# Kernel tuning notes

Hardware: AMD Instinct MI355X
Metric: run time of the kernel (lower is better)

The kernel has to match this reference:

```python
import jax, jax.numpy as jnp
import numpy as np

N_NODES = 100_000
N_EDGES = 1_200_000


def _lap_weights(src, dst, attr, n):
    # PyG get_laplacian(sym) + ChebConv scaling with lambda_max=2.0:
    # L_hat = (2/lmax)(I - D^-1/2 A D^-1/2) - I = -D^-1/2 A D^-1/2 (zero diagonal)
    deg = jnp.zeros((n,), attr.dtype).at[src].add(attr)
    dis = jnp.where(deg > 0, jax.lax.rsqrt(jnp.maximum(deg, 1e-30)), 0.0)
    return -(dis[src] * attr * dis[dst])


def _prop(x, src, dst, lw, n):
    # y_i = sum_{(j->i)} lw_e * x_j   (gather -> scale -> scatter-add)
    return jnp.zeros((n, x.shape[1]), x.dtype).at[dst].add(lw[:, None] * x[src])


def _cheb(x, src, dst, lw, W, b):
    # W: [K, F_in, F_out]; Tx0 = x, Tx1 = L_hat x (K<=2 here)
    out = x @ W[0]
    if W.shape[0] > 1:
        tx1 = _prop(x, src, dst, lw, x.shape[0])
        out = out + tx1 @ W[1]
    return out + b


def setup_inputs() -> dict:
    key = jax.random.key(0)
    ks = jax.random.split(key, 11)
    x = jax.random.normal(ks[0], (N_NODES, 20), jnp.float32)
    edge_index = jax.random.randint(ks[1], (2, N_EDGES), 0, N_NODES, jnp.int32)
    attr = jax.random.uniform(ks[2], (N_EDGES,), jnp.float32)
    def glorot(k, shape):
        fan = shape[-2] + shape[-1]
        return jax.random.normal(k, shape, jnp.float32) * jnp.sqrt(2.0 / fan)
    return {
        "x": x, "edge_index": edge_index, "attr": attr,
        "w1": glorot(ks[3], (1, 20, 32)), "b1": jnp.zeros((32,), jnp.float32),
        "w2": glorot(ks[4], (2, 32, 64)), "b2": jnp.zeros((64,), jnp.float32),
        "w3": glorot(ks[5], (2, 64, 2)), "b3": jnp.zeros((2,), jnp.float32),
        "gate_w": glorot(ks[6], (2, 1)), "gate_b": jnp.zeros((1,), jnp.float32),
    }


def reference(x, edge_index, attr, w1, b1, w2, b2, w3, b3, gate_w, gate_b):
    n = x.shape[0]
    src, dst = edge_index[0], edge_index[1]
    lw = _lap_weights(src, dst, attr, n)
    h = jax.nn.leaky_relu(_cheb(x, src, dst, lw, w1, b1))   # [N, 32]
    h = jax.nn.leaky_relu(_cheb(h, src, dst, lw, w2, b2))   # [N, 64]
    h = _cheb(h, src, dst, lw, w3, b3)                       # [N, 2]
    # GlobalAttention with batch = zeros (single graph): softmax over nodes
    gate = jax.nn.softmax(h @ gate_w + gate_b, axis=0)       # [N, 1]
    pooled = jnp.sum(gate * h, axis=0, keepdims=True)        # [1, 2]
    return jax.nn.log_softmax(pooled, axis=1)
```

## Files before the change

kernel.cpp:

```cpp
#include <hip/hip_runtime.h>
#include <hip/hip_bf16.h>
#include <math.h>

#define N_NODES 100000
#define N_EDGES 1200000
#define E4 (N_EDGES / 4)
#define G2B ((N_NODES + 255) / 256)
#define NB_L1 G2B
#define RANGE 12800
#define NRANGE 8
#define CHK 32
#define NB_DEG (NRANGE * CHK)
#define GPC ((E4 + CHK - 1) / CHK)
#define NBIN 391
#define BINCAP 3584
#define NB_P1 256
#define GP1 ((E4 + NB_P1 - 1) / NB_P1)

__device__ __forceinline__ float disf(float d) {
    return (d > 0.f) ? rsqrtf(d) : 0.f;
}
__device__ __forceinline__ unsigned packe(int s, float w) {
    unsigned q = (unsigned)(w * 32767.f + 0.5f);
    return ((unsigned)s << 15) | q;
}
__device__ __forceinline__ void unpacke(unsigned p, int& s, float& w) {
    s = (int)(p >> 15);
    w = (float)(p & 0x7FFFu) * (1.f / 32767.f);
}

__global__ void degbin_kernel(const int4* __restrict__ src4, const float4* __restrict__ attr4,
                              float* __restrict__ partial) {
    __shared__ float ldeg[RANGE];
    int rb = blockIdx.x;
    int r = rb / CHK;
    int c = rb - r * CHK;
    int base = r * RANGE;
    for (int j = threadIdx.x; j < RANGE; j += blockDim.x) ldeg[j] = 0.f;
    __syncthreads();
    int g0 = c * GPC;
    int g1 = g0 + GPC; if (g1 > E4) g1 = E4;
    for (int g = g0 + threadIdx.x; g < g1; g += blockDim.x) {
        int4 s = src4[g];
        float4 a = attr4[g];
        unsigned o;
        o = (unsigned)(s.x - base); if (o < RANGE) atomicAdd(&ldeg[o], a.x);
        o = (unsigned)(s.y - base); if (o < RANGE) atomicAdd(&ldeg[o], a.y);
        o = (unsigned)(s.z - base); if (o < RANGE) atomicAdd(&ldeg[o], a.z);
        o = (unsigned)(s.w - base); if (o < RANGE) atomicAdd(&ldeg[o], a.w);
    }
    __syncthreads();
    float* dstp = partial + (size_t)rb * RANGE;
    for (int j = threadIdx.x; j < RANGE; j += blockDim.x) dstp[j] = ldeg[j];
}

__global__ void degred_kernel(const float* __restrict__ partial, float* __restrict__ deg) {
    int i = blockIdx.x * blockDim.x + threadIdx.x;
    if (i >= N_NODES) return;
    int r = i / RANGE;
    int j = i - r * RANGE;
    const float* p = partial + (size_t)r * CHK * RANGE + j;
    float s = 0.f;
#pragma unroll
    for (int c = 0; c < CHK; c++) s += p[(size_t)c * RANGE];
    deg[i] = s;
}

__global__ void p1l1_kernel(const int4* __restrict__ src4, const int4* __restrict__ dst4,
                            const float4* __restrict__ attr4, const float* __restrict__ deg,
                            const float* __restrict__ x, const float* __restrict__ w1,
                            const float* __restrict__ b1,
                            int* __restrict__ binCursor, uint2* __restrict__ binRegion,
                            signed char* __restrict__ h1q, float* __restrict__ sscale) {
    __shared__ int lhist[NBIN];
    __shared__ int lbase[NBIN];
    __shared__ int lcnt[NBIN];
    __shared__ float sw[20 * 32];
    __shared__ float sb[32];

    if (blockIdx.x < NB_P1) {
        int g0 = blockIdx.x * GP1;
        int g1 = g0 + GP1; if (g1 > E4) g1 = E4;
        for (int j = threadIdx.x; j < NBIN; j += blockDim.x) { lhist[j] = 0; lcnt[j] = 0; }
        __syncthreads();
        for (int g = g0 + threadIdx.x; g < g1; g += blockDim.x) {
            int4 d = dst4[g];
            atomicAdd(&lhist[d.x >> 8], 1);
            atomicAdd(&lhist[d.y >> 8], 1);
            atomicAdd(&lhist[d.z >> 8], 1);
            atomicAdd(&lhist[d.w >> 8], 1);
        }
        __syncthreads();
        for (int j = threadIdx.x; j < NBIN; j += blockDim.x)
            lbase[j] = (lhist[j] > 0) ? atomicAdd(&binCursor[j], lhist[j]) : 0;
        __syncthreads();
        for (int g = g0 + threadIdx.x; g < g1; g += blockDim.x) {
            int4 s = src4[g];
            int4 d = dst4[g];
            float4 a = attr4[g];
            {
                int bin = d.x >> 8;
                float w = a.x * disf(deg[s.x]);
                int pos = lbase[bin] + atomicAdd(&lcnt[bin], 1);
                if (pos < BINCAP)
                    binRegion[(size_t)bin * BINCAP + pos] =
                        make_uint2(((unsigned)s.x << 8) | (unsigned)(d.x & 255), __float_as_uint(w));
            }
            {
                int bin = d.y >> 8;
                float w = a.y * disf(deg[s.y]);
                int pos = lbase[bin] + atomicAdd(&lcnt[bin], 1);
                if (pos < BINCAP)
                    binRegion[(size_t)bin * BINCAP + pos] =
                        make_uint2(((unsigned)s.y << 8) | (unsigned)(d.y & 255), __float_as_uint(w));
            }
            {
                int bin = d.z >> 8;
                float w = a.z * disf(deg[s.z]);
                int pos = lbase[bin] + atomicAdd(&lcnt[bin], 1);
                if (pos < BINCAP)
                    binRegion[(size_t)bin * BINCAP + pos] =
                        make_uint2(((unsigned)s.z << 8) | (unsigned)(d.z & 255), __float_as_uint(w));
            }
            {
                int bin = d.w >> 8;
                float w = a.w * disf(deg[s.w]);
                int pos = lbase[bin] + atomicAdd(&lcnt[bin], 1);
                if (pos < BINCAP)
                    binRegion[(size_t)bin * BINCAP + pos] =
                        make_uint2(((unsigned)s.w << 8) | (unsigned)(d.w & 255), __float_as_uint(w));
            }
        }
    } else {
        for (int t = threadIdx.x; t < 20 * 32; t += blockDim.x) sw[t] = w1[t];
        if (threadIdx.x < 32) sb[threadIdx.x] = b1[threadIdx.x];
        __syncthreads();
        int i = (blockIdx.x - NB_P1) * blockDim.x + threadIdx.x;
        if (i >= N_NODES) return;
        float xr[20];
#pragma unroll
        for (int k = 0; k < 20; k++) xr[k] = x[(size_t)i * 20 + k];
        float row[32];
        float rmax = 0.f;
#pragma unroll
        for (int j = 0; j < 32; j++) {
            float a = sb[j];
#pragma unroll
            for (int k = 0; k < 20; k++) a += xr[k] * sw[k * 32 + j];
            a = (a > 0.f) ? a : 0.01f * a;
            row[j] = a;
            rmax = fmaxf(rmax, fabsf(a));
        }
        float sc = (rmax > 0.f) ? rmax * (1.f / 127.f) : 1.f;
        float inv = (rmax > 0.f) ? 127.f / rmax : 0.f;
        sscale[i] = sc;
#pragma unroll
        for (int j = 0; j < 32; j++) {
            float q = row[j] * inv;
            h1q[(size_t)i * 32 + j] = (signed char)lrintf(q);
        }
    }
}

__global__ void binscan_kernel(const int* __restrict__ binCursor, int* __restrict__ bin_start) {
    __shared__ int sm[512];
    int t = threadIdx.x;
    int v = 0;
    if (t < NBIN) {
        v = binCursor[t];
        if (v > BINCAP) v = BINCAP;
    }
    sm[t] = v;
    __syncthreads();
    for (int off = 1; off < 512; off <<= 1) {
        int u = (t >= off) ? sm[t - off] : 0;
        __syncthreads();
        sm[t] += u;
        __syncthreads();
    }
    if (t < NBIN) bin_start[t + 1] = sm[t];
    if (t == 0) bin_start[0] = 0;
}

__global__ void p2_kernel(const uint2* __restrict__ binRegion, const int* __restrict__ bin_start,
                          int* __restrict__ row_start, unsigned* __restrict__ csr) {
    __shared__ uint2 recs[BINCAP];
    __shared__ int hist[256];
    __shared__ int excl[256];
    __shared__ int cnt[256];
    int b = blockIdx.x;
    int t = threadIdx.x;
    int base = bin_start[b];
    int c = bin_start[b + 1] - base;
    const uint2* reg = binRegion + (size_t)b * BINCAP;
    for (int j = t; j < c; j += 256) recs[j] = reg[j];
    hist[t] = 0; cnt[t] = 0;
    __syncthreads();
    for (int j = t; j < c; j += 256) atomicAdd(&hist[recs[j].x & 255u], 1);
    __syncthreads();
    int v = hist[t];
    excl[t] = v;
    __syncthreads();
    for (int off = 1; off < 256; off <<= 1) {
        int u = (t >= off) ? excl[t - off] : 0;
        __syncthreads();
        excl[t] += u;
        __syncthreads();
    }
    int ex = excl[t] - v;
    row_start[b * 256 + t] = base + ex;
    if (b == NBIN - 1 && t == 255) row_start[NBIN * 256] = bin_start[NBIN];
    __syncthreads();
    hist[t] = ex;
    __syncthreads();
    for (int j = t; j < c; j += 256) {
        unsigned w0 = recs[j].x;
        int low = (int)(w0 & 255u);
        int src = (int)(w0 >> 8);
        float w = __uint_as_float(recs[j].y);
        int pos = hist[low] + atomicAdd(&cnt[low], 1);
        csr[base + pos] = packe(src, w);
    }
}

__global__ void gl2_kernel(const int* __restrict__ row_start, const unsigned* __restrict__ csr,
                           const float* __restrict__ deg, const signed char* __restrict__ h1q,
                           const float* __restrict__ sscale,
                           const float* __restrict__ w2, const float* __restrict__ b2,
                           const float* __restrict__ w3,
                           float2* __restrict__ z0, float2* __restrict__ z1) {
    __shared__ float s0[32 * 64];
    __shared__ float s1[32 * 64];
    __shared__ float sw3[256];
    __shared__ float sb[64];
    __shared__ float h1s[8][32];
    __shared__ float t1s[8][32];
    for (int t = threadIdx.x; t < 32 * 64; t += blockDim.x) {
        s0[t] = w2[t];
        s1[t] = w2[32 * 64 + t];
    }
    for (int t = threadIdx.x; t < 256; t += blockDim.x) sw3[t] = w3[t];
    if (threadIdx.x < 64) sb[threadIdx.x] = b2[threadIdx.x];
    __syncthreads();

    int grp = threadIdx.x >> 5;
    int f   = threadIdx.x & 31;
    int node = blockIdx.x * 8 + grp;
    bool alive = (node < N_NODES);

    if (alive) {
        float hv = sscale[node] * (float)h1q[(size_t)node * 32 + f];
        int rs = row_start[node], re = row_start[node + 1];
        float acc0 = 0.f, acc1 = 0.f;
        int j = rs;
        for (; j + 1 < re; j += 2) {
            unsigned e0 = csr[j], e1 = csr[j + 1];
            int sa, sbi; float w0, w1v;
            unpacke(e0, sa, w0);
            unpacke(e1, sbi, w1v);
            float ws0 = w0 * sscale[sa];
            float ws1 = w1v * sscale[sbi];
            acc0 += ws0 * (float)h1q[(size_t)sa * 32 + f];
            acc1 += ws1 * (float)h1q[(size_t)sbi * 32 + f];
        }
        if (j < re) {
            unsigned e0 = csr[j];
            int sa; float w0;
            unpacke(e0, sa, w0);
            acc0 += w0 * sscale[sa] * (float)h1q[(size_t)sa * 32 + f];
        }
        h1s[grp][f] = hv;
        t1s[grp][f] = -disf(deg[node]) * (acc0 + acc1);
    }
    __syncthreads();

    float a0 = sb[f], a1 = sb[f + 32];
#pragma unroll 8
    for (int k = 0; k < 32; k++) {
        float h = h1s[grp][k];
        float tv = t1s[grp][k];
        a0 += h * s0[k * 64 + f]      + tv * s1[k * 64 + f];
        a1 += h * s0[k * 64 + f + 32] + tv * s1[k * 64 + f + 32];
    }
    float v0 = (a0 > 0.f) ? a0 : 0.01f * a0;
    float v1 = (a1 > 0.f) ? a1 : 0.01f * a1;

    float z00 = v0 * sw3[f * 2 + 0] + v1 * sw3[(f + 32) * 2 + 0];
    float z01 = v0 * sw3[f * 2 + 1] + v1 * sw3[(f + 32) * 2 + 1];
    float z10 = v0 * sw3[128 + f * 2 + 0] + v1 * sw3[128 + (f + 32) * 2 + 0];
    float z11 = v0 * sw3[128 + f * 2 + 1] + v1 * sw3[128 + (f + 32) * 2 + 1];
#pragma unroll
    for (int m = 16; m > 0; m >>= 1) {
        z00 += __shfl_xor(z00, m);
        z01 += __shfl_xor(z01, m);
        z10 += __shfl_xor(z10, m);
        z11 += __shfl_xor(z11, m);
    }
    if (alive && f == 0) {
        z0[node] = make_float2(z00, z01);
        z1[node] = make_float2(z10, z11);
    }
}

__global__ void g2acc_kernel(const int* __restrict__ row_start, const unsigned* __restrict__ csr,
                             const float* __restrict__ deg,
                             const float2* __restrict__ z0, const float2* __restrict__ z1,
                             const float* __restrict__ b3, const float* __restrict__ gw,
                             const float* __restrict__ gb, float4* __restrict__ quads) {
    __shared__ float sm[256], ss[256], s0[256], s1[256];
    int t = threadIdx.x;
    int i = blockIdx.x * blockDim.x + t;
    float m = -INFINITY, se = 0.f, a0 = 0.f, a1 = 0.f;
    if (i < N_NODES) {
        int rs = row_start[i], re = row_start[i + 1];
        float acc0 = 0.f, acc1 = 0.f;
        for (int j = rs; j < re; j++) {
            int s; float w;
            unpacke(csr[j], s, w);
            float2 zv = z1[s];
            acc0 += w * zv.x;
            acc1 += w * zv.y;
        }
        float di = -disf(deg[i]);
        float2 z0v = z0[i];
        float o0 = z0v.x + di * acc0 + b3[0];
        float o1 = z0v.y + di * acc1 + b3[1];
        m = o0 * gw[0] + o1 * gw[1] + gb[0];
        se = 1.f; a0 = o0; a1 = o1;
    }
    sm[t] = m; ss[t] = se; s0[t] = a0; s1[t] = a1;
    __syncthreads();
    for (int s = 128; s > 0; s >>= 1) {
        if (t < s) {
            float mb = sm[t + s];
            if (mb != -INFINITY) {
                float ma = sm[t];
                if (ma == -INFINITY) {
                    sm[t] = mb; ss[t] = ss[t + s]; s0[t] = s0[t + s]; s1[t] = s1[t + s];
                } else if (mb <= ma) {
                    float c = __expf(mb - ma);
                    ss[t] += ss[t + s] * c;
                    s0[t] += s0[t + s] * c;
                    s1[t] += s1[t + s] * c;
                } else {
                    float c = __expf(ma - mb);
                    ss[t] = ss[t] * c + ss[t + s];
                    s0[t] = s0[t] * c + s0[t + s];
                    s1[t] = s1[t] * c + s1[t + s];
                    sm[t] = mb;
                }
            }
        }
        __syncthreads();
    }
    if (t == 0) quads[blockIdx.x] = make_float4(sm[0], ss[0], s0[0], s1[0]);
}

__global__ void accB_kernel(const float4* __restrict__ quads, float* __restrict__ out) {
    __shared__ float sm[512], ss[512], s0[512], s1[512];
    int t = threadIdx.x;
    float m = -INFINITY, se = 0.f, a0 = 0.f, a1 = 0.f;
    if (t < G2B) {
        float4 q = quads[t];
        m = q.x; se = q.y; a0 = q.z; a1 = q.w;
    }
    sm[t] = m; ss[t] = se; s0[t] = a0; s1[t] = a1;
    __syncthreads();
    for (int s = 256; s > 0; s >>= 1) {
        if (t < s) {
            float mb = sm[t + s];
            if (mb != -INFINITY) {
                float ma = sm[t];
                if (ma == -INFINITY) {
                    sm[t] = mb; ss[t] = ss[t + s]; s0[t] = s0[t + s]; s1[t] = s1[t + s];
                } else if (mb <= ma) {
                    float c = __expf(mb - ma);
                    ss[t] += ss[t + s] * c;
                    s0[t] += s0[t + s] * c;
                    s1[t] += s1[t + s] * c;
                } else {
                    float c = __expf(ma - mb);
                    ss[t] = ss[t] * c + ss[t + s];
                    s0[t] = s0[t] * c + s0[t + s];
                    s1[t] = s1[t] * c + s1[t + s];
                    sm[t] = mb;
                }
            }
        }
        __syncthreads();
    }
    if (t == 0) {
        float se0 = ss[0];
        float p0 = s0[0] / se0;
        float p1 = s1[0] / se0;
        float mm = fmaxf(p0, p1);
        float l = mm + logf(__expf(p0 - mm) + __expf(p1 - mm));
        out[0] = p0 - l;
        out[1] = p1 - l;
    }
}

extern "C" void kernel_launch(void* const* d_in, const int* in_sizes, int n_in,
                              void* d_out, int out_size, void* d_ws, size_t ws_size,
                              hipStream_t stream) {
    const float* x    = (const float*)d_in[0];
    const int*   ei   = (const int*)d_in[1];
    const float* attr = (const float*)d_in[2];
    const float* w1   = (const float*)d_in[3];
    const float* b1   = (const float*)d_in[4];
    const float* w2   = (const float*)d_in[5];
    const float* b2   = (const float*)d_in[6];
    const float* w3   = (const float*)d_in[7];
    const float* b3   = (const float*)d_in[8];
    const float* gw   = (const float*)d_in[9];
    const float* gb   = (const float*)d_in[10];
    float* out = (float*)d_out;

    const int4*   src4  = (const int4*)ei;
    const int4*   dst4  = (const int4*)(ei + N_EDGES);
    const float4* attr4 = (const float4*)attr;

    float* ws = (float*)d_ws;
    size_t off = 0;
    int*      binCursor = (int*)(ws + off); off += NBIN;
    int*      bin_start = (int*)(ws + off); off += NBIN + 1;
    float*    deg       = ws + off; off += N_NODES;
    float*    sscale    = ws + off; off += N_NODES;
    int*      row_start = (int*)(ws + off); off += NBIN * 256 + 1;
    float*    partial   = ws + off; off += (size_t)NB_DEG * RANGE;
    off = (off + 3) & ~(size_t)3;
    uint2*    binRegion = (uint2*)(ws + off); off += (size_t)NBIN * BINCAP * 2;
    unsigned* csr       = (unsigned*)(ws + off); off += N_EDGES;
    signed char* h1q    = (signed char*)(ws + off); off += (size_t)N_NODES * 8;
    float2*   z0  = (float2*)(ws + off); off += (size_t)N_NODES * 2;
    float2*   z1  = (float2*)(ws + off); off += (size_t)N_NODES * 2;
    off = (off + 3) & ~(size_t)3;
    float4*   quads = (float4*)(ws + off); off += (size_t)G2B * 4;

    const int B = 256;
    auto cdiv = [](long long a, long long b) { return (int)((a + b - 1) / b); };

    hipMemsetAsync(binCursor, 0, NBIN * sizeof(int), stream);

    degbin_kernel<<<NB_DEG, B, 0, stream>>>(src4, attr4, partial);
    degred_kernel<<<cdiv(N_NODES, B), B, 0, stream>>>(partial, deg);

    p1l1_kernel<<<NB_P1 + NB_L1, B, 0, stream>>>(src4, dst4, attr4, deg, x, w1, b1,
                                                 binCursor, binRegion, h1q, sscale);

    binscan_kernel<<<1, 512, 0, stream>>>(binCursor, bin_start);

    p2_kernel<<<NBIN, B, 0, stream>>>(binRegion, bin_start, row_start, csr);

    gl2_kernel<<<cdiv(N_NODES, 8), B, 0, stream>>>(row_start, csr, deg, h1q, sscale,
                                                   w2, b2, w3, z0, z1);

    g2acc_kernel<<<G2B, B, 0, stream>>>(row_start, csr, deg, z0, z1, b3, gw, gb, quads);

    accB_kernel<<<1, 512, 0, stream>>>(quads, out);
}
```

Baseline: 175.0 us.

## Fold source scale into quantized edge weights and use integer gather-accumulate

The per-source int8 scale is multiplied into the edge weight when the CSR is built, and the product is quantized to 15 bits. Layer-2 aggregation can then run as integer multiply-accumulate with no per-edge sscale gather. The gather is also restructured so four lanes split the edges and each lane loads 4 packed int8 features as one int, with a shuffle reduction at the end. Layer 3 divides z1 by the node scale so the shared quantized weights still apply. The costs are extra quantization error and clamping from the larger WQ factor, plus a possible loss of precision in z1w when a node's scale is tiny.

```diff
diff --git a/kernel.cpp b/kernel.cpp
--- a/kernel.cpp
+++ b/kernel.cpp
@@ -16,17 +16,10 @@
 #define BINCAP 3584
 #define NB_P1 256
 #define GP1 ((E4 + NB_P1 - 1) / NB_P1)
+#define WQ (8.f * 32767.f)
 
 __device__ __forceinline__ float disf(float d) {
     return (d > 0.f) ? rsqrtf(d) : 0.f;
-}
-__device__ __forceinline__ unsigned packe(int s, float w) {
-    unsigned q = (unsigned)(w * 32767.f + 0.5f);
-    return ((unsigned)s << 15) | q;
-}
-__device__ __forceinline__ void unpacke(unsigned p, int& s, float& w) {
-    s = (int)(p >> 15);
-    w = (float)(p & 0x7FFFu) * (1.f / 32767.f);
 }
 
 __global__ void degbin_kernel(const int4* __restrict__ src4, const float4* __restrict__ attr4,
@@ -151,13 +144,12 @@
             row[j] = a;
             rmax = fmaxf(rmax, fabsf(a));
         }
-        float sc = (rmax > 0.f) ? rmax * (1.f / 127.f) : 1.f;
-        float inv = (rmax > 0.f) ? 127.f / rmax : 0.f;
+        float sc = fmaxf(rmax * (1.f / 127.f), 1e-4f);
+        float inv = 1.f / sc;
         sscale[i] = sc;
 #pragma unroll
         for (int j = 0; j < 32; j++) {
-            float q = row[j] * inv;
-            h1q[(size_t)i * 32 + j] = (signed char)lrintf(q);
+            h1q[(size_t)i * 32 + j] = (signed char)lrintf(row[j] * inv);
         }
     }
 }
@@ -183,6 +175,7 @@
 }
 
 __global__ void p2_kernel(const uint2* __restrict__ binRegion, const int* __restrict__ bin_start,
+                          const float* __restrict__ sscale,
                           int* __restrict__ row_start, unsigned* __restrict__ csr) {
     __shared__ uint2 recs[BINCAP];
     __shared__ int hist[256];
@@ -218,8 +211,11 @@
         int low = (int)(w0 & 255u);
         int src = (int)(w0 >> 8);
         float w = __uint_as_float(recs[j].y);
+        float ws = w * sscale[src] * WQ;
+        unsigned q = (unsigned)(ws + 0.5f);
+        if (q > 32767u) q = 32767u;
         int pos = hist[low] + atomicAdd(&cnt[low], 1);
-        csr[base + pos] = packe(src, w);
+        csr[base + pos] = ((unsigned)src << 15) | q;
     }
 }
 
@@ -228,7 +224,7 @@
                            const float* __restrict__ sscale,
                            const float* __restrict__ w2, const float* __restrict__ b2,
                            const float* __restrict__ w3,
-                           float2* __restrict__ z0, float2* __restrict__ z1) {
+                           float2* __restrict__ z0, float2* __restrict__ z1w) {
     __shared__ float s0[32 * 64];
     __shared__ float s1[32 * 64];
     __shared__ float sw3[256];
@@ -244,36 +240,47 @@
     __syncthreads();
 
     int grp = threadIdx.x >> 5;
-    int f   = threadIdx.x & 31;
+    int lane = threadIdx.x & 31;
+    int e4 = lane >> 3;
+    int fg = lane & 7;
     int node = blockIdx.x * 8 + grp;
     bool alive = (node < N_NODES);
 
+    int acc0 = 0, acc1 = 0, acc2 = 0, acc3 = 0;
     if (alive) {
-        float hv = sscale[node] * (float)h1q[(size_t)node * 32 + f];
         int rs = row_start[node], re = row_start[node + 1];
-        float acc0 = 0.f, acc1 = 0.f;
-        int j = rs;
-        for (; j + 1 < re; j += 2) {
-            unsigned e0 = csr[j], e1 = csr[j + 1];
-            int sa, sbi; float w0, w1v;
-            unpacke(e0, sa, w0);
-            unpacke(e1, sbi, w1v);
-            float ws0 = w0 * sscale[sa];
-            float ws1 = w1v * sscale[sbi];
-            acc0 += ws0 * (float)h1q[(size_t)sa * 32 + f];
-            acc1 += ws1 * (float)h1q[(size_t)sbi * 32 + f];
-        }
-        if (j < re) {
-            unsigned e0 = csr[j];
-            int sa; float w0;
-            unpacke(e0, sa, w0);
-            acc0 += w0 * sscale[sa] * (float)h1q[(size_t)sa * 32 + f];
-        }
-        h1s[grp][f] = hv;
-        t1s[grp][f] = -disf(deg[node]) * (acc0 + acc1);
-    }
-    __syncthreads();
-
+        for (int j = rs + e4; j < re; j += 4) {
+            unsigned e = csr[j];
+            int sa = (int)(e >> 15);
+            int wq = (int)(e & 0x7FFFu);
+            int packed = *reinterpret_cast<const int*>(h1q + (size_t)sa * 32 + fg * 4);
+            acc0 += wq * (int)(signed char)(packed);
+            acc1 += wq * (int)(signed char)(packed >> 8);
+            acc2 += wq * (int)(signed char)(packed >> 16);
+            acc3 += wq * (int)(signed char)(packed >> 24);
+        }
+    }
+    acc0 += __shfl_xor(acc0, 8);  acc0 += __shfl_xor(acc0, 16);
+    acc1 += __shfl_xor(acc1, 8);  acc1 += __shfl_xor(acc1, 16);
+    acc2 += __shfl_xor(acc2, 8);  acc2 += __shfl_xor(acc2, 16);
+    acc3 += __shfl_xor(acc3, 8);  acc3 += __shfl_xor(acc3, 16);
+
+    if (alive && e4 == 0) {
+        float dn = -disf(deg[node]) * (1.f / WQ);
+        int packed = *reinterpret_cast<const int*>(h1q + (size_t)node * 32 + fg * 4);
+        float sc = sscale[node];
+        h1s[grp][fg * 4 + 0] = sc * (float)(signed char)(packed);
+        h1s[grp][fg * 4 + 1] = sc * (float)(signed char)(packed >> 8);
+        h1s[grp][fg * 4 + 2] = sc * (float)(signed char)(packed >> 16);
+        h1s[grp][fg * 4 + 3] = sc * (float)(signed char)(packed >> 24);
+        t1s[grp][fg * 4 + 0] = dn * (float)acc0;
+        t1s[grp][fg * 4 + 1] = dn * (float)acc1;
+        t1s[grp][fg * 4 + 2] = dn * (float)acc2;
+        t1s[grp][fg * 4 + 3] = dn * (float)acc3;
+    }
+    __syncthreads();
+
+    int f = lane;
     float a0 = sb[f], a1 = sb[f + 32];
 #pragma unroll 8
     for (int k = 0; k < 32; k++) {
@@ -298,13 +305,14 @@
     }
     if (alive && f == 0) {
         z0[node] = make_float2(z00, z01);
-        z1[node] = make_float2(z10, z11);
+        float isc = 1.f / sscale[node];
+        z1w[node] = make_float2(z10 * isc, z11 * isc);
     }
 }
 
 __global__ void g2acc_kernel(const int* __restrict__ row_start, const unsigned* __restrict__ csr,
                              const float* __restrict__ deg,
-                             const float2* __restrict__ z0, const float2* __restrict__ z1,
+                             const float2* __restrict__ z0, const float2* __restrict__ z1w,
                              const float* __restrict__ b3, const float* __restrict__ gw,
                              const float* __restrict__ gb, float4* __restrict__ quads) {
     __shared__ float sm[256], ss[256], s0[256], s1[256];
@@ -315,13 +323,14 @@
         int rs = row_start[i], re = row_start[i + 1];
         float acc0 = 0.f, acc1 = 0.f;
         for (int j = rs; j < re; j++) {
-            int s; float w;
-            unpacke(csr[j], s, w);
-            float2 zv = z1[s];
-            acc0 += w * zv.x;
-            acc1 += w * zv.y;
-        }
-        float di = -disf(deg[i]);
+            unsigned e = csr[j];
+            int s = (int)(e >> 15);
+            float wq = (float)(e & 0x7FFFu);
+            float2 zv = z1w[s];
+            acc0 += wq * zv.x;
+            acc1 += wq * zv.y;
+        }
+        float di = -disf(deg[i]) * (1.f / WQ);
         float2 z0v = z0[i];
         float o0 = z0v.x + di * acc0 + b3[0];
         float o1 = z0v.y + di * acc1 + b3[1];
@@ -433,7 +442,7 @@
     unsigned* csr       = (unsigned*)(ws + off); off += N_EDGES;
     signed char* h1q    = (signed char*)(ws + off); off += (size_t)N_NODES * 8;
     float2*   z0  = (float2*)(ws + off); off += (size_t)N_NODES * 2;
-    float2*   z1  = (float2*)(ws + off); off += (size_t)N_NODES * 2;
+    float2*   z1w = (float2*)(ws + off); off += (size_t)N_NODES * 2;
     off = (off + 3) & ~(size_t)3;
     float4*   quads = (float4*)(ws + off); off += (size_t)G2B * 4;
 
@@ -450,12 +459,12 @@
 
     binscan_kernel<<<1, 512, 0, stream>>>(binCursor, bin_start);
 
-    p2_kernel<<<NBIN, B, 0, stream>>>(binRegion, bin_start, row_start, csr);
+    p2_kernel<<<NBIN, B, 0, stream>>>(binRegion, bin_start, sscale, row_start, csr);
 
     gl2_kernel<<<cdiv(N_NODES, 8), B, 0, stream>>>(row_start, csr, deg, h1q, sscale,
-                                                   w2, b2, w3, z0, z1);
-
-    g2acc_kernel<<<G2B, B, 0, stream>>>(row_start, csr, deg, z0, z1, b3, gw, gb, quads);
+                                                   w2, b2, w3, z0, z1w);
+
+    g2acc_kernel<<<G2B, B, 0, stream>>>(row_start, csr, deg, z0, z1w, b3, gw, gb, quads);
 
     accB_kernel<<<1, 512, 0, stream>>>(quads, out);
 }
```

After: 162.4 us. 1.08x faster.

## Drop CSR build and aggregate per bin with shared-memory integer atomics

Applied to the files above, without the earlier changes.

Removes the bin-scan and per-bin CSR sort kernels. The layer-2 and layer-3 aggregation kernels now read the unsorted per-bin edge records directly and scatter-add into per-block shared-memory accumulators. Layer 2 uses quantized int atomics on an int8 feature times a fixed-point weight. Chunk counts for the degree and binning passes are also doubled. This saves two launches and a full CSR write/read, at the cost of heavy LDS atomic traffic, a large shared footprint that limits occupancy, and fixed-point rounding changes.

```diff
diff --git a/kernel.cpp b/kernel.cpp
--- a/kernel.cpp
+++ b/kernel.cpp
@@ -5,28 +5,21 @@
 #define N_NODES 100000
 #define N_EDGES 1200000
 #define E4 (N_EDGES / 4)
-#define G2B ((N_NODES + 255) / 256)
-#define NB_L1 G2B
+#define NB_L1 ((N_NODES + 255) / 256)
 #define RANGE 12800
 #define NRANGE 8
-#define CHK 32
+#define CHK 64
 #define NB_DEG (NRANGE * CHK)
 #define GPC ((E4 + CHK - 1) / CHK)
 #define NBIN 391
 #define BINCAP 3584
-#define NB_P1 256
+#define NB_P1 512
 #define GP1 ((E4 + NB_P1 - 1) / NB_P1)
+#define WQ (8.f * 32767.f)
+#define GLX_T 512
 
 __device__ __forceinline__ float disf(float d) {
     return (d > 0.f) ? rsqrtf(d) : 0.f;
-}
-__device__ __forceinline__ unsigned packe(int s, float w) {
-    unsigned q = (unsigned)(w * 32767.f + 0.5f);
-    return ((unsigned)s << 15) | q;
-}
-__device__ __forceinline__ void unpacke(unsigned p, int& s, float& w) {
-    s = (int)(p >> 15);
-    w = (float)(p & 0x7FFFu) * (1.f / 32767.f);
 }
 
 __global__ void degbin_kernel(const int4* __restrict__ src4, const float4* __restrict__ attr4,
@@ -151,81 +144,19 @@
             row[j] = a;
             rmax = fmaxf(rmax, fabsf(a));
         }
-        float sc = (rmax > 0.f) ? rmax * (1.f / 127.f) : 1.f;
-        float inv = (rmax > 0.f) ? 127.f / rmax : 0.f;
+        float sc = fmaxf(rmax * (1.f / 127.f), 1e-4f);
+        float inv = 1.f / sc;
         sscale[i] = sc;
 #pragma unroll
         for (int j = 0; j < 32; j++) {
-            float q = row[j] * inv;
-            h1q[(size_t)i * 32 + j] = (signed char)lrintf(q);
-        }
-    }
-}
-
-__global__ void binscan_kernel(const int* __restrict__ binCursor, int* __restrict__ bin_start) {
-    __shared__ int sm[512];
-    int t = threadIdx.x;
-    int v = 0;
-    if (t < NBIN) {
-        v = binCursor[t];
-        if (v > BINCAP) v = BINCAP;
-    }
-    sm[t] = v;
-    __syncthreads();
-    for (int off = 1; off < 512; off <<= 1) {
-        int u = (t >= off) ? sm[t - off] : 0;
-        __syncthreads();
-        sm[t] += u;
-        __syncthreads();
-    }
-    if (t < NBIN) bin_start[t + 1] = sm[t];
-    if (t == 0) bin_start[0] = 0;
-}
-
-__global__ void p2_kernel(const uint2* __restrict__ binRegion, const int* __restrict__ bin_start,
-                          int* __restrict__ row_start, unsigned* __restrict__ csr) {
-    __shared__ uint2 recs[BINCAP];
-    __shared__ int hist[256];
-    __shared__ int excl[256];
-    __shared__ int cnt[256];
-    int b = blockIdx.x;
-    int t = threadIdx.x;
-    int base = bin_start[b];
-    int c = bin_start[b + 1] - base;
-    const uint2* reg = binRegion + (size_t)b * BINCAP;
-    for (int j = t; j < c; j += 256) recs[j] = reg[j];
-    hist[t] = 0; cnt[t] = 0;
-    __syncthreads();
-    for (int j = t; j < c; j += 256) atomicAdd(&hist[recs[j].x & 255u], 1);
-    __syncthreads();
-    int v = hist[t];
-    excl[t] = v;
-    __syncthreads();
-    for (int off = 1; off < 256; off <<= 1) {
-        int u = (t >= off) ? excl[t - off] : 0;
-        __syncthreads();
-        excl[t] += u;
-        __syncthreads();
-    }
-    int ex = excl[t] - v;
-    row_start[b * 256 + t] = base + ex;
-    if (b == NBIN - 1 && t == 255) row_start[NBIN * 256] = bin_start[NBIN];
-    __syncthreads();
-    hist[t] = ex;
-    __syncthreads();
-    for (int j = t; j < c; j += 256) {
-        unsigned w0 = recs[j].x;
-        int low = (int)(w0 & 255u);
-        int src = (int)(w0 >> 8);
-        float w = __uint_as_float(recs[j].y);
-        int pos = hist[low] + atomicAdd(&cnt[low], 1);
-        csr[base + pos] = packe(src, w);
-    }
-}
-
-__global__ void gl2_kernel(const int* __restrict__ row_start, const unsigned* __restrict__ csr,
-                           const float* __restrict__ deg, const signed char* __restrict__ h1q,
-                           const float* __restrict__ sscale,
+            h1q[(size_t)i * 32 + j] = (signed char)lrintf(row[j] * inv);
+        }
+    }
+}
+
+__global__ void glx_kernel(const int* __restrict__ binCursor, const uint2* __restrict__ binRegion,
+                           const float* __restrict__ deg, const float* __restrict__ sscale,
+                           const signed char* __restrict__ h1q,
                            const float* __restrict__ w2, const float* __restrict__ b2,
                            const float* __restrict__ w3,
                            float2* __restrict__ z0, float2* __restrict__ z1) {
@@ -233,134 +164,153 @@
     __shared__ float s1[32 * 64];
     __shared__ float sw3[256];
     __shared__ float sb[64];
-    __shared__ float h1s[8][32];
-    __shared__ float t1s[8][32];
-    for (int t = threadIdx.x; t < 32 * 64; t += blockDim.x) {
-        s0[t] = w2[t];
-        s1[t] = w2[32 * 64 + t];
-    }
-    for (int t = threadIdx.x; t < 256; t += blockDim.x) sw3[t] = w3[t];
-    if (threadIdx.x < 64) sb[threadIdx.x] = b2[threadIdx.x];
-    __syncthreads();
-
-    int grp = threadIdx.x >> 5;
-    int f   = threadIdx.x & 31;
-    int node = blockIdx.x * 8 + grp;
-    bool alive = (node < N_NODES);
-
-    if (alive) {
-        float hv = sscale[node] * (float)h1q[(size_t)node * 32 + f];
-        int rs = row_start[node], re = row_start[node + 1];
-        float acc0 = 0.f, acc1 = 0.f;
-        int j = rs;
-        for (; j + 1 < re; j += 2) {
-            unsigned e0 = csr[j], e1 = csr[j + 1];
-            int sa, sbi; float w0, w1v;
-            unpacke(e0, sa, w0);
-            unpacke(e1, sbi, w1v);
-            float ws0 = w0 * sscale[sa];
-            float ws1 = w1v * sscale[sbi];
-            acc0 += ws0 * (float)h1q[(size_t)sa * 32 + f];
-            acc1 += ws1 * (float)h1q[(size_t)sbi * 32 + f];
-        }
-        if (j < re) {
-            unsigned e0 = csr[j];
-            int sa; float w0;
-            unpacke(e0, sa, w0);
-            acc0 += w0 * sscale[sa] * (float)h1q[(size_t)sa * 32 + f];
-        }
-        h1s[grp][f] = hv;
-        t1s[grp][f] = -disf(deg[node]) * (acc0 + acc1);
-    }
-    __syncthreads();
-
-    float a0 = sb[f], a1 = sb[f + 32];
+    __shared__ int   t1acc[256][33];
+    __shared__ float hf[8][32];
+    __shared__ float tf[8][32];
+    int b = blockIdx.x, tid = threadIdx.x;
+
+    for (int t = tid; t < 32 * 64; t += GLX_T) { s0[t] = w2[t]; s1[t] = w2[2048 + t]; }
+    for (int t = tid; t < 256; t += GLX_T) sw3[t] = w3[t];
+    if (tid < 64) sb[tid] = b2[tid];
+    int* tz = &t1acc[0][0];
+    for (int t = tid; t < 256 * 33; t += GLX_T) tz[t] = 0;
+    __syncthreads();
+
+    int cnt = binCursor[b]; if (cnt > BINCAP) cnt = BINCAP;
+    const uint2* reg = binRegion + (size_t)b * BINCAP;
+    for (int r = tid; r < cnt; r += GLX_T) {
+        uint2 rec = reg[r];
+        int src = (int)(rec.x >> 8);
+        int dl  = (int)(rec.x & 255u);
+        float w = __uint_as_float(rec.y);
+        float ws = w * sscale[src] * WQ;
+        int wq = (int)(ws + 0.5f);
+        if (wq > 32767) wq = 32767;
+        const int4* hp = reinterpret_cast<const int4*>(h1q + (size_t)src * 32);
+        int4 A = hp[0];
+        int4 B = hp[1];
+        int* arow = t1acc[dl];
+#define ACC4(d, base) \
+        atomicAdd(&arow[(base)+0], __mul24(wq, (int)(signed char)((d)      ))); \
+        atomicAdd(&arow[(base)+1], __mul24(wq, (int)(signed char)((d) >>  8))); \
+        atomicAdd(&arow[(base)+2], __mul24(wq, (int)(signed char)((d) >> 16))); \
+        atomicAdd(&arow[(base)+3], __mul24(wq, (int)(signed char)((d) >> 24)));
+        ACC4(A.x, 0)  ACC4(A.y, 4)  ACC4(A.z, 8)  ACC4(A.w, 12)
+        ACC4(B.x, 16) ACC4(B.y, 20) ACC4(B.z, 24) ACC4(B.w, 28)
+#undef ACC4
+    }
+    __syncthreads();
+
+    int ns = tid >> 6;
+    int f  = tid & 63;
+    for (int bat = 0; bat < 32; ++bat) {
+        if (tid < 256) {
+            int nsS = tid >> 5, k = tid & 31;
+            int dl = bat * 8 + nsS;
+            int node = b * 256 + dl;
+            if (node < N_NODES) {
+                float sc = sscale[node];
+                hf[nsS][k] = sc * (float)(signed char)h1q[(size_t)node * 32 + k];
+                float dn = -disf(deg[node]) * (1.f / WQ);
+                tf[nsS][k] = dn * (float)t1acc[dl][k];
+            }
+        }
+        __syncthreads();
+        int node = b * 256 + bat * 8 + ns;
+        if (node < N_NODES) {
+            float a = sb[f];
 #pragma unroll 8
-    for (int k = 0; k < 32; k++) {
-        float h = h1s[grp][k];
-        float tv = t1s[grp][k];
-        a0 += h * s0[k * 64 + f]      + tv * s1[k * 64 + f];
-        a1 += h * s0[k * 64 + f + 32] + tv * s1[k * 64 + f + 32];
-    }
-    float v0 = (a0 > 0.f) ? a0 : 0.01f * a0;
-    float v1 = (a1 > 0.f) ? a1 : 0.01f * a1;
-
-    float z00 = v0 * sw3[f * 2 + 0] + v1 * sw3[(f + 32) * 2 + 0];
-    float z01 = v0 * sw3[f * 2 + 1] + v1 * sw3[(f + 32) * 2 + 1];
-    float z10 = v0 * sw3[128 + f * 2 + 0] + v1 * sw3[128 + (f + 32) * 2 + 0];
-    float z11 = v0 * sw3[128 + f * 2 + 1] + v1 * sw3[128 + (f + 32) * 2 + 1];
-#pragma unroll
-    for (int m = 16; m > 0; m >>= 1) {
-        z00 += __shfl_xor(z00, m);
-        z01 += __shfl_xor(z01, m);
-        z10 += __shfl_xor(z10, m);
-        z11 += __shfl_xor(z11, m);
-    }
-    if (alive && f == 0) {
-        z0[node] = make_float2(z00, z01);
-        z1[node] = make_float2(z10, z11);
-    }
-}
-
-__global__ void g2acc_kernel(const int* __restrict__ row_start, const unsigned* __restrict__ csr,
+            for (int k = 0; k < 32; ++k)
+                a += hf[ns][k] * s0[k * 64 + f] + tf[ns][k] * s1[k * 64 + f];
+            float v = (a > 0.f) ? a : 0.01f * a;
+            float z00 = v * sw3[f * 2 + 0];
+            float z01 = v * sw3[f * 2 + 1];
+            float z10 = v * sw3[128 + f * 2 + 0];
+            float z11 = v * sw3[128 + f * 2 + 1];
+#pragma unroll
+            for (int m = 32; m > 0; m >>= 1) {
+                z00 += __shfl_xor(z00, m);
+                z01 += __shfl_xor(z01, m);
+                z10 += __shfl_xor(z10, m);
+                z11 += __shfl_xor(z11, m);
+            }
+            if (f == 0) {
+                z0[node] = make_float2(z00, z01);
+                z1[node] = make_float2(z10, z11);
+            }
+        }
+        __syncthreads();
+    }
+}
+
+__global__ void gaccx_kernel(const int* __restrict__ binCursor, const uint2* __restrict__ binRegion,
                              const float* __restrict__ deg,
                              const float2* __restrict__ z0, const float2* __restrict__ z1,
                              const float* __restrict__ b3, const float* __restrict__ gw,
                              const float* __restrict__ gb, float4* __restrict__ quads) {
-    __shared__ float sm[256], ss[256], s0[256], s1[256];
-    int t = threadIdx.x;
-    int i = blockIdx.x * blockDim.x + t;
+    __shared__ float acc2[256][2];
+    __shared__ float sm[512], ss[512], s0s[512], s1s[512];
+    int b = blockIdx.x, tid = threadIdx.x;
+    float* az = &acc2[0][0];
+    for (int t = tid; t < 512; t += 512) az[t] = 0.f;
+    __syncthreads();
+    int cnt = binCursor[b]; if (cnt > BINCAP) cnt = BINCAP;
+    const uint2* reg = binRegion + (size_t)b * BINCAP;
+    for (int r = tid; r < cnt; r += 512) {
+        uint2 rec = reg[r];
+        int src = (int)(rec.x >> 8);
+        int dl  = (int)(rec.x & 255u);
+        float w = __uint_as_float(rec.y);
+        float2 zv = z1[src];
+        atomicAdd(&acc2[dl][0], w * zv.x);
+        atomicAdd(&acc2[dl][1], w * zv.y);
+    }
+    __syncthreads();
     float m = -INFINITY, se = 0.f, a0 = 0.f, a1 = 0.f;
-    if (i < N_NODES) {
-        int rs = row_start[i], re = row_start[i + 1];
-        float acc0 = 0.f, acc1 = 0.f;
-        for (int j = rs; j < re; j++) {
-            int s; float w;
-            unpacke(csr[j], s, w);
-            float2 zv = z1[s];
-            acc0 += w * zv.x;
-            acc1 += w * zv.y;
-        }
-        float di = -disf(deg[i]);
-        float2 z0v = z0[i];
-        float o0 = z0v.x + di * acc0 + b3[0];
-        float o1 = z0v.y + di * acc1 + b3[1];
-        m = o0 * gw[0] + o1 * gw[1] + gb[0];
-        se = 1.f; a0 = o0; a1 = o1;
-    }
-    sm[t] = m; ss[t] = se; s0[t] = a0; s1[t] = a1;
-    __syncthreads();
-    for (int s = 128; s > 0; s >>= 1) {
-        if (t < s) {
-            float mb = sm[t + s];
+    if (tid < 256) {
+        int node = b * 256 + tid;
+        if (node < N_NODES) {
+            float di = -disf(deg[node]);
+            float2 zz = z0[node];
+            float o0 = zz.x + di * acc2[tid][0] + b3[0];
+            float o1 = zz.y + di * acc2[tid][1] + b3[1];
+            m = o0 * gw[0] + o1 * gw[1] + gb[0];
+            se = 1.f; a0 = o0; a1 = o1;
+        }
+    }
+    sm[tid] = m; ss[tid] = se; s0s[tid] = a0; s1s[tid] = a1;
+    __syncthreads();
+    for (int s = 256; s > 0; s >>= 1) {
+        if (tid < s) {
+            float mb = sm[tid + s];
             if (mb != -INFINITY) {
-                float ma = sm[t];
+                float ma = sm[tid];
                 if (ma == -INFINITY) {
-                    sm[t] = mb; ss[t] = ss[t + s]; s0[t] = s0[t + s]; s1[t] = s1[t + s];
+                    sm[tid] = mb; ss[tid] = ss[tid + s]; s0s[tid] = s0s[tid + s]; s1s[tid] = s1s[tid + s];
                 } else if (mb <= ma) {
                     float c = __expf(mb - ma);
-                    ss[t] += ss[t + s] * c;
-                    s0[t] += s0[t + s] * c;
-                    s1[t] += s1[t + s] * c;
+                    ss[tid] += ss[tid + s] * c;
+                    s0s[tid] += s0s[tid + s] * c;
+                    s1s[tid] += s1s[tid + s] * c;
                 } else {
                     float c = __expf(ma - mb);
-                    ss[t] = ss[t] * c + ss[t + s];
-                    s0[t] = s0[t] * c + s0[t + s];
-                    s1[t] = s1[t] * c + s1[t + s];
-                    sm[t] = mb;
+                    ss[tid] = ss[tid] * c + ss[tid + s];
+                    s0s[tid] = s0s[tid] * c + s0s[tid + s];
+                    s1s[tid] = s1s[tid] * c + s1s[tid + s];
+                    sm[tid] = mb;
                 }
             }
         }
         __syncthreads();
     }
-    if (t == 0) quads[blockIdx.x] = make_float4(sm[0], ss[0], s0[0], s1[0]);
+    if (tid == 0) quads[b] = make_float4(sm[0], ss[0], s0s[0], s1s[0]);
 }
 
 __global__ void accB_kernel(const float4* __restrict__ quads, float* __restrict__ out) {
     __shared__ float sm[512], ss[512], s0[512], s1[512];
     int t = threadIdx.x;
     float m = -INFINITY, se = 0.f, a0 = 0.f, a1 = 0.f;
-    if (t < G2B) {
+    if (t < NBIN) {
         float4 q = quads[t];
         m = q.x; se = q.y; a0 = q.z; a1 = q.w;
     }
@@ -423,19 +373,16 @@
     float* ws = (float*)d_ws;
     size_t off = 0;
     int*      binCursor = (int*)(ws + off); off += NBIN;
-    int*      bin_start = (int*)(ws + off); off += NBIN + 1;
     float*    deg       = ws + off; off += N_NODES;
     float*    sscale    = ws + off; off += N_NODES;
-    int*      row_start = (int*)(ws + off); off += NBIN * 256 + 1;
+    off = (off + 3) & ~(size_t)3;
     float*    partial   = ws + off; off += (size_t)NB_DEG * RANGE;
-    off = (off + 3) & ~(size_t)3;
     uint2*    binRegion = (uint2*)(ws + off); off += (size_t)NBIN * BINCAP * 2;
-    unsigned* csr       = (unsigned*)(ws + off); off += N_EDGES;
     signed char* h1q    = (signed char*)(ws + off); off += (size_t)N_NODES * 8;
     float2*   z0  = (float2*)(ws + off); off += (size_t)N_NODES * 2;
     float2*   z1  = (float2*)(ws + off); off += (size_t)N_NODES * 2;
     off = (off + 3) & ~(size_t)3;
-    float4*   quads = (float4*)(ws + off); off += (size_t)G2B * 4;
+    float4*   quads = (float4*)(ws + off); off += (size_t)NBIN * 4;
 
     const int B = 256;
     auto cdiv = [](long long a, long long b) { return (int)((a + b - 1) / b); };
@@ -448,14 +395,11 @@
     p1l1_kernel<<<NB_P1 + NB_L1, B, 0, stream>>>(src4, dst4, attr4, deg, x, w1, b1,
                                                  binCursor, binRegion, h1q, sscale);
 
-    binscan_kernel<<<1, 512, 0, stream>>>(binCursor, bin_start);
-
-    p2_kernel<<<NBIN, B, 0, stream>>>(binRegion, bin_start, row_start, csr);
-
-    gl2_kernel<<<cdiv(N_NODES, 8), B, 0, stream>>>(row_start, csr, deg, h1q, sscale,
-                                                   w2, b2, w3, z0, z1);
-
-    g2acc_kernel<<<G2B, B, 0, stream>>>(row_start, csr, deg, z0, z1, b3, gw, gb, quads);
+    glx_kernel<<<NBIN, GLX_T, 0, stream>>>(binCursor, binRegion, deg, sscale, h1q,
+                                           w2, b2, w3, z0, z1);
+
+    gaccx_kernel<<<NBIN, 512, 0, stream>>>(binCursor, binRegion, deg, z0, z1,
+                                           b3, gw, gb, quads);
 
     accB_kernel<<<1, 512, 0, stream>>>(quads, out);
 }
```

Measured after the change: 212.0 us. +21.1%, slower.
